# Kernel tuning notes

Measured on AMD Instinct MI355X. Metric: run time of the kernel, lower is better.

## Reference

```python
import jax, jax.numpy as jnp
import numpy as np

B, N, C = 16, 256, 2048
CLASSES = (16, 5, 5)
H = len(CLASSES)
EPS = 1e-5


def setup_inputs() -> dict:
    key = jax.random.key(0)
    ks = iter(jax.random.split(key, 32))
    d = {}
    d["features"] = jax.random.normal(next(ks), (B, N, C), dtype=jnp.float32)
    # 3 hidden conv layers per head; 3x3 conv on 1x1 spatial == linear with center tap.
    # Stack the H heads' weights: [H, C_out, C_in].
    std = 1.0 / np.sqrt(C)
    for i in (1, 2, 3):
        d[f"W{i}"] = jax.random.normal(next(ks), (H, C, C), dtype=jnp.float32) * std
        d[f"g{i}"] = 1.0 + 0.1 * jax.random.normal(next(ks), (H, C), dtype=jnp.float32)
        d[f"b{i}"] = 0.1 * jax.random.normal(next(ks), (H, C), dtype=jnp.float32)
        d[f"m{i}"] = 0.1 * jax.random.normal(next(ks), (H, C), dtype=jnp.float32)
        d[f"v{i}"] = jax.random.uniform(next(ks), (H, C), dtype=jnp.float32, minval=0.5, maxval=1.5)
    # Final 1x1 conv per head: [c_i, C] weight + [c_i] bias (output dims differ per head).
    for h, c in enumerate(CLASSES):
        d[f"Wf{h}"] = jax.random.normal(next(ks), (c, C), dtype=jnp.float32) * std
        d[f"bf{h}"] = 0.1 * jax.random.normal(next(ks), (c,), dtype=jnp.float32)
    return d


def _bn_relu(y, g, b, m, v):
    # y: [H, M, C]; per-head inference-mode BN folded to scale/shift, then ReLU.
    scale = g / jnp.sqrt(v + EPS)          # [H, C]
    shift = b - m * scale                  # [H, C]
    return jax.nn.relu(y * scale[:, None, :] + shift[:, None, :])


def reference(features, W1, g1, b1, m1, v1, W2, g2, b2, m2, v2, W3, g3, b3, m3, v3,
              Wf0, bf0, Wf1, bf1, Wf2, bf2):
    Bs, Ns, Cs = features.shape
    x = features.reshape(Bs * Ns, Cs)                       # [M, C]
    y = jnp.einsum("mc,hdc->hmd", x, W1)                    # [H, M, C]
    y = _bn_relu(y, g1, b1, m1, v1)
    y = jnp.einsum("hmc,hdc->hmd", y, W2)
    y = _bn_relu(y, g2, b2, m2, v2)
    y = jnp.einsum("hmc,hdc->hmd", y, W3)
    y = _bn_relu(y, g3, b3, m3, v3)
    outs = [y[h] @ Wf.T + bf for h, (Wf, bf) in enumerate([(Wf0, bf0), (Wf1, bf1), (Wf2, bf2)])]
    cl = jnp.concatenate(outs, axis=-1)                     # [M, sum(classes)]
    return cl.reshape(Bs, Ns, cl.shape[-1])
```

## Files before the change

### kernel.cpp

```cpp
#include <hip/hip_runtime.h>
#include <hip/hip_bf16.h>

typedef __attribute__((ext_vector_type(8))) short short8;
typedef __attribute__((ext_vector_type(4))) float f32x4;

#define BN_EPS 1e-5f
#define MROWS 4096
#define CDIM 2048

#define SB() __builtin_amdgcn_sched_barrier(0)

__device__ __forceinline__ void gload_lds16(const void* g, void* l) {
  __builtin_amdgcn_global_load_lds(
      (const __attribute__((address_space(1))) void*)g,
      (__attribute__((address_space(3))) void*)l, 16, 0, 0);
}

__global__ __launch_bounds__(256) void cvt_f32_bf16(const float* __restrict__ in,
                                                    unsigned short* __restrict__ out,
                                                    int n4) {
  int idx = blockIdx.x * blockDim.x + threadIdx.x;
  int stride = gridDim.x * blockDim.x;
  for (int i = idx; i < n4; i += stride) {
    float4 vv = ((const float4*)in)[i];
    __hip_bfloat16 h0 = __float2bfloat16(vv.x);
    __hip_bfloat16 h1 = __float2bfloat16(vv.y);
    __hip_bfloat16 h2 = __float2bfloat16(vv.z);
    __hip_bfloat16 h3 = __float2bfloat16(vv.w);
    ushort4 o;
    o.x = *(unsigned short*)&h0;
    o.y = *(unsigned short*)&h1;
    o.z = *(unsigned short*)&h2;
    o.w = *(unsigned short*)&h3;
    ((ushort4*)out)[i] = o;
  }
}

__global__ __launch_bounds__(512, 4) void gemm128_bn_relu(
    const __hip_bfloat16* __restrict__ A, long long a_hstride,
    const __hip_bfloat16* __restrict__ W,
    const float* __restrict__ gp, const float* __restrict__ bp,
    const float* __restrict__ mp, const float* __restrict__ vp,
    __hip_bfloat16* __restrict__ out)
{
  __shared__ __hip_bfloat16 sm[36864];

  const int tid  = threadIdx.x;
  const int w    = tid >> 6;
  const int lane = tid & 63;

  const int bid = blockIdx.x;
  const int swz = (bid & 7) * 96 + (bid >> 3);
  const int h   = swz >> 8;
  const int rem = swz & 255;
  const int mt  = rem >> 3;
  const int nt  = rem & 7;

  const __hip_bfloat16* Abase = A + (size_t)h * (size_t)a_hstride + (size_t)(mt * 128) * CDIM;
  const __hip_bfloat16* Bbase = W + ((size_t)h * CDIM + (size_t)(nt * 256)) * CDIM;

  const int rowA = tid >> 2;
  const int chA  = (tid & 3) ^ ((rowA >> 1) & 3);
  const __hip_bfloat16* aSrc  = Abase + (size_t)rowA * CDIM + chA * 8;
  const __hip_bfloat16* bSrc0 = Bbase + (size_t)rowA * CDIM + chA * 8;
  const __hip_bfloat16* bSrc1 = bSrc0 + (size_t)128 * CDIM;

  const int wm = w >> 2, wn = w & 3;
  const int fr = lane & 15, fg = lane >> 4;
  const int cadj  = (fg ^ ((fr >> 1) & 3)) * 8;
  const int abase = (wm * 64 + fr) * 32 + cadj;
  const int bbase = 4096 + (wn * 64 + fr) * 32 + cadj;

  auto STAGE = [&](int off, int t) {
    __hip_bfloat16* dp = &sm[off + tid * 8];
    gload_lds16(aSrc  + t * 32, dp);
    gload_lds16(bSrc0 + t * 32, dp + 4096);
    gload_lds16(bSrc1 + t * 32, dp + 8192);
  };

  f32x4 acc[4][4] = {};

  STAGE(0, 0);
  STAGE(12288, 1);
  asm volatile("s_waitcnt vmcnt(3)" ::: "memory");
  SB();
  __builtin_amdgcn_s_barrier();
  SB();

  int oc = 0, on = 12288, os = 24576;
  for (int t = 0; t < 64; ++t) {
    if (t + 2 < 64) STAGE(os, t + 2);
    SB();
    short8 af[4], bf_[4];
#pragma unroll
    for (int i = 0; i < 4; ++i) af[i]  = *(const short8*)&sm[oc + abase + i * 512];
#pragma unroll
    for (int j = 0; j < 4; ++j) bf_[j] = *(const short8*)&sm[oc + bbase + j * 512];
    __builtin_amdgcn_s_setprio(1);
#pragma unroll
    for (int i = 0; i < 4; ++i)
#pragma unroll
      for (int j = 0; j < 4; ++j)
        acc[i][j] = __builtin_amdgcn_mfma_f32_16x16x32_bf16(af[i], bf_[j], acc[i][j], 0, 0, 0);
    __builtin_amdgcn_s_setprio(0);
    SB();
    if (t < 63) {
      if (t + 2 < 64) { asm volatile("s_waitcnt vmcnt(3)" ::: "memory"); }
      else            { asm volatile("s_waitcnt vmcnt(0)" ::: "memory"); }
      SB();
      __builtin_amdgcn_s_barrier();
      SB();
    }
    const int tmp = oc; oc = on; on = os; os = tmp;
  }

  const float* gh = gp + h * CDIM;
  const float* bh = bp + h * CDIM;
  const float* mh = mp + h * CDIM;
  const float* vh = vp + h * CDIM;
  const int colBase = nt * 256 + wn * 64 + fr;
  const int rowBase = mt * 128 + wm * 64 + fg * 4;
#pragma unroll
  for (int j = 0; j < 4; ++j) {
    const int col = colBase + j * 16;
    const float sc = gh[col] / sqrtf(vh[col] + BN_EPS);
    const float sh = bh[col] - mh[col] * sc;
#pragma unroll
    for (int i = 0; i < 4; ++i) {
      const int row = rowBase + i * 16;
#pragma unroll
      for (int rr = 0; rr < 4; ++rr) {
        float val = acc[i][j][rr] * sc + sh;
        val = val > 0.f ? val : 0.f;
        out[((size_t)h * MROWS + row + rr) * CDIM + col] = __float2bfloat16(val);
      }
    }
  }
}

__global__ __launch_bounds__(256) void pack_wf(
    const float* __restrict__ Wf0, const float* __restrict__ Wf1,
    const float* __restrict__ Wf2, __hip_bfloat16* __restrict__ Wfb) {
  int idx = blockIdx.x * 256 + threadIdx.x;
  if (idx >= 3 * 16 * CDIM) return;
  int h = idx / (16 * CDIM);
  int rem = idx - h * 16 * CDIM;
  int j = rem / CDIM;
  int k = rem - j * CDIM;
  float v = 0.f;
  if (h == 0)            v = Wf0[j * CDIM + k];
  else if (h == 1)       { if (j < 5) v = Wf1[j * CDIM + k]; }
  else                   { if (j < 5) v = Wf2[j * CDIM + k]; }
  Wfb[idx] = __float2bfloat16(v);
}

__global__ __launch_bounds__(512) void final_mfma(
    const __hip_bfloat16* __restrict__ act,
    const __hip_bfloat16* __restrict__ Wfb,
    const float* __restrict__ bf0, const float* __restrict__ bf1,
    const float* __restrict__ bf2, float* __restrict__ out)
{
  __shared__ float red[8][3][256];
  const int tid  = threadIdx.x;
  const int w    = tid >> 6;
  const int lane = tid & 63;
  const int r0   = blockIdx.x * 16;
  const int fr   = lane & 15;
  const int fk   = (lane >> 4) * 8;
  const int kbase = w * 256 + fk;

  f32x4 acc[3] = {};
  const __hip_bfloat16* aRow = act + (size_t)(r0 + fr) * CDIM + kbase;
  const __hip_bfloat16* bRow = Wfb + (size_t)fr * CDIM + kbase;
#pragma unroll
  for (int ks = 0; ks < 8; ++ks) {
    const int k = ks * 32;
#pragma unroll
    for (int h = 0; h < 3; ++h) {
      short8 a = *(const short8*)(aRow + (size_t)h * MROWS * CDIM + k);
      short8 b = *(const short8*)(bRow + h * 16 * CDIM + k);
      acc[h] = __builtin_amdgcn_mfma_f32_16x16x32_bf16(a, b, acc[h], 0, 0, 0);
    }
  }

  const int rb = (lane >> 4) * 4;
#pragma unroll
  for (int h = 0; h < 3; ++h)
#pragma unroll
    for (int r = 0; r < 4; ++r)
      red[w][h][(rb + r) * 16 + fr] = acc[h][r];
  __syncthreads();

  for (int e = tid; e < 768; e += 512) {
    const int h = e >> 8, idx = e & 255;
    const int row = idx >> 4, col = idx & 15;
    float s = 0.f;
#pragma unroll
    for (int w2 = 0; w2 < 8; ++w2) s += red[w2][h][idx];
    float* orow = out + (size_t)(r0 + row) * 26;
    if (h == 0)                 orow[col]      = s + bf0[col];
    else if (h == 1) { if (col < 5) orow[16 + col] = s + bf1[col]; }
    else             { if (col < 5) orow[21 + col] = s + bf2[col]; }
  }
}

extern "C" void kernel_launch(void* const* d_in, const int* in_sizes, int n_in,
                              void* d_out, int out_size, void* d_ws, size_t ws_size,
                              hipStream_t stream) {
  const float* feat = (const float*)d_in[0];
  const float* W1 = (const float*)d_in[1];
  const float* g1 = (const float*)d_in[2];
  const float* b1 = (const float*)d_in[3];
  const float* m1 = (const float*)d_in[4];
  const float* v1 = (const float*)d_in[5];
  const float* W2 = (const float*)d_in[6];
  const float* g2 = (const float*)d_in[7];
  const float* b2 = (const float*)d_in[8];
  const float* m2 = (const float*)d_in[9];
  const float* v2 = (const float*)d_in[10];
  const float* W3 = (const float*)d_in[11];
  const float* g3 = (const float*)d_in[12];
  const float* b3 = (const float*)d_in[13];
  const float* m3 = (const float*)d_in[14];
  const float* v3 = (const float*)d_in[15];
  const float* Wf0 = (const float*)d_in[16];
  const float* bf0 = (const float*)d_in[17];
  const float* Wf1 = (const float*)d_in[18];
  const float* bf1 = (const float*)d_in[19];
  const float* Wf2 = (const float*)d_in[20];
  const float* bf2 = (const float*)d_in[21];
  float* out = (float*)d_out;

  char* ws = (char*)d_ws;
  __hip_bfloat16* wbuf = (__hip_bfloat16*)ws;
  __hip_bfloat16* actA = (__hip_bfloat16*)(ws + 25165824);
  __hip_bfloat16* actB = (__hip_bfloat16*)(ws + 25165824 + 50331648);
  __hip_bfloat16* xb   = actB;
  __hip_bfloat16* Wfb  = wbuf;

  const int nW4 = (3 * CDIM * CDIM) / 4;
  const int nX4 = (MROWS * CDIM) / 4;
  const long long hstride = (long long)MROWS * CDIM;

  cvt_f32_bf16<<<2048, 256, 0, stream>>>(feat, (unsigned short*)xb, nX4);

  cvt_f32_bf16<<<2048, 256, 0, stream>>>(W1, (unsigned short*)wbuf, nW4);
  gemm128_bn_relu<<<768, 512, 0, stream>>>(xb, 0LL, wbuf, g1, b1, m1, v1, actA);

  cvt_f32_bf16<<<2048, 256, 0, stream>>>(W2, (unsigned short*)wbuf, nW4);
  gemm128_bn_relu<<<768, 512, 0, stream>>>(actA, hstride, wbuf, g2, b2, m2, v2, actB);

  cvt_f32_bf16<<<2048, 256, 0, stream>>>(W3, (unsigned short*)wbuf, nW4);
  gemm128_bn_relu<<<768, 512, 0, stream>>>(actB, hstride, wbuf, g3, b3, m3, v3, actA);

  pack_wf<<<384, 256, 0, stream>>>(Wf0, Wf1, Wf2, Wfb);
  final_mfma<<<256, 512, 0, stream>>>(actA, Wfb, bf0, bf1, bf2, out);
}
```

Measured before the change: 389.8 us.

## Widen GEMM K-tile to 64 and interleave LDS fragment loads with MFMA

The main bf16 GEMM now stages K-tiles of 64 instead of 32, which halves the number of barrier iterations, and it uses a new XOR swizzle for the 64-wide rows. Within each iteration the work is split into four MFMA groups, with LDS fragment reads and global-to-LDS prefetches placed between them so data movement overlaps compute. The next tile's first fragments are loaded right after the barrier. In exchange, LDS use doubles to 144 KB per block and the occupancy hint drops to 2 blocks per CU, so fewer waves are resident to hide latency.

```diff
diff --git a/kernel.cpp b/kernel.cpp
--- a/kernel.cpp
+++ b/kernel.cpp
@@ -7,6 +7,7 @@
 #define BN_EPS 1e-5f
 #define MROWS 4096
 #define CDIM 2048
+#define NKT 32
 
 #define SB() __builtin_amdgcn_sched_barrier(0)
 
@@ -36,14 +37,14 @@
   }
 }
 
-__global__ __launch_bounds__(512, 4) void gemm128_bn_relu(
+__global__ __launch_bounds__(512, 2) void gemm128_ring(
     const __hip_bfloat16* __restrict__ A, long long a_hstride,
     const __hip_bfloat16* __restrict__ W,
     const float* __restrict__ gp, const float* __restrict__ bp,
     const float* __restrict__ mp, const float* __restrict__ vp,
     __hip_bfloat16* __restrict__ out)
 {
-  __shared__ __hip_bfloat16 sm[36864];
+  __shared__ __hip_bfloat16 sm[73728];
 
   const int tid  = threadIdx.x;
   const int w    = tid >> 6;
@@ -59,56 +60,89 @@
   const __hip_bfloat16* Abase = A + (size_t)h * (size_t)a_hstride + (size_t)(mt * 128) * CDIM;
   const __hip_bfloat16* Bbase = W + ((size_t)h * CDIM + (size_t)(nt * 256)) * CDIM;
 
-  const int rowA = tid >> 2;
-  const int chA  = (tid & 3) ^ ((rowA >> 1) & 3);
-  const __hip_bfloat16* aSrc  = Abase + (size_t)rowA * CDIM + chA * 8;
-  const __hip_bfloat16* bSrc0 = Bbase + (size_t)rowA * CDIM + chA * 8;
-  const __hip_bfloat16* bSrc1 = bSrc0 + (size_t)128 * CDIM;
+  const int row0 = tid >> 3;
+  const int ch0  = (tid & 7) ^ (row0 & 7);
+  const __hip_bfloat16* aSrc = Abase + (size_t)row0 * CDIM + ch0 * 8;
+  const __hip_bfloat16* bSrc = Bbase + (size_t)row0 * CDIM + ch0 * 8;
 
   const int wm = w >> 2, wn = w & 3;
   const int fr = lane & 15, fg = lane >> 4;
-  const int cadj  = (fg ^ ((fr >> 1) & 3)) * 8;
-  const int abase = (wm * 64 + fr) * 32 + cadj;
-  const int bbase = 4096 + (wn * 64 + fr) * 32 + cadj;
-
-  auto STAGE = [&](int off, int t) {
-    __hip_bfloat16* dp = &sm[off + tid * 8];
-    gload_lds16(aSrc  + t * 32, dp);
-    gload_lds16(bSrc0 + t * 32, dp + 4096);
-    gload_lds16(bSrc1 + t * 32, dp + 8192);
+  const int offs0 = fr * 64 + ((fg ^ (fr & 7)) << 3);
+  const int offs1 = fr * 64 + (((fg + 4) ^ (fr & 7)) << 3);
+  const int aoffs0 = wm * 4096 + offs0;
+  const int aoffs1 = wm * 4096 + offs1;
+  const int boffs0 = 8192 + wn * 4096 + offs0;
+  const int boffs1 = 8192 + wn * 4096 + offs1;
+
+  auto SA = [&](int buf, int t) {
+    __hip_bfloat16* dp = &sm[buf + tid * 8];
+    gload_lds16(aSrc + t * 64, dp);
+    gload_lds16(aSrc + (size_t)64 * CDIM + t * 64, dp + 4096);
   };
+  auto SB0 = [&](int buf, int t) {
+    __hip_bfloat16* dp = &sm[buf + 8192 + tid * 8];
+    gload_lds16(bSrc + t * 64, dp);
+    gload_lds16(bSrc + (size_t)64 * CDIM + t * 64, dp + 4096);
+  };
+  auto SB1 = [&](int buf, int t) {
+    __hip_bfloat16* dp = &sm[buf + 8192 + 8192 + tid * 8];
+    gload_lds16(bSrc + (size_t)128 * CDIM + t * 64, dp);
+    gload_lds16(bSrc + (size_t)192 * CDIM + t * 64, dp + 4096);
+  };
 
   f32x4 acc[4][4] = {};
-
-  STAGE(0, 0);
-  STAGE(12288, 1);
-  asm volatile("s_waitcnt vmcnt(3)" ::: "memory");
+  short8 Af[4], Ap[4], B0[2], B1[2], B0p[2], B1p[2];
+
+#define LDA4(dst, base)                                                  \
+  _Pragma("unroll") for (int i_ = 0; i_ < 4; ++i_)                       \
+    dst[i_] = *(const short8*)&sm[(base) + i_ * 1024];
+#define LDB2(dst, base, j0)                                              \
+  _Pragma("unroll") for (int j_ = 0; j_ < 2; ++j_)                       \
+    dst[j_] = *(const short8*)&sm[(base) + ((j0) + j_) * 1024];
+
+#define MFMA_G(joff, Aset, Bset)                                         \
+  __builtin_amdgcn_s_setprio(1);                                         \
+  _Pragma("unroll") for (int i_ = 0; i_ < 4; ++i_)                       \
+  _Pragma("unroll") for (int j_ = 0; j_ < 2; ++j_)                       \
+    acc[i_][j_ + joff] = __builtin_amdgcn_mfma_f32_16x16x32_bf16(        \
+        Aset[i_], Bset[j_], acc[i_][j_ + joff], 0, 0, 0);                \
+  __builtin_amdgcn_s_setprio(0);
+
+  SA(0, 0); SB0(0, 0); SB1(0, 0);
+  SA(24576, 1); SB0(24576, 1); SB1(24576, 1);
+  asm volatile("s_waitcnt vmcnt(6)" ::: "memory");
   SB();
   __builtin_amdgcn_s_barrier();
   SB();
-
-  int oc = 0, on = 12288, os = 24576;
-  for (int t = 0; t < 64; ++t) {
-    if (t + 2 < 64) STAGE(os, t + 2);
+  LDA4(Af, 0 + aoffs0);
+  LDB2(B0, 0 + boffs0, 0);
+  LDB2(B1, 0 + boffs0, 2);
+  SB();
+
+  int oc = 0, on = 24576, os = 49152;
+  for (int t = 0; t < NKT; ++t) {
+    MFMA_G(0, Af, B0); SB();
+    LDB2(B0p, oc + boffs1, 0); SB();
+    MFMA_G(2, Af, B1); SB();
+    LDA4(Ap, oc + aoffs1);
+    if (t + 2 < NKT) SA(os, t + 2);
     SB();
-    short8 af[4], bf_[4];
-#pragma unroll
-    for (int i = 0; i < 4; ++i) af[i]  = *(const short8*)&sm[oc + abase + i * 512];
-#pragma unroll
-    for (int j = 0; j < 4; ++j) bf_[j] = *(const short8*)&sm[oc + bbase + j * 512];
-    __builtin_amdgcn_s_setprio(1);
-#pragma unroll
-    for (int i = 0; i < 4; ++i)
-#pragma unroll
-      for (int j = 0; j < 4; ++j)
-        acc[i][j] = __builtin_amdgcn_mfma_f32_16x16x32_bf16(af[i], bf_[j], acc[i][j], 0, 0, 0);
-    __builtin_amdgcn_s_setprio(0);
+    MFMA_G(0, Ap, B0p); SB();
+    LDB2(B1p, oc + boffs1, 2);
+    if (t + 2 < NKT) SB0(os, t + 2);
     SB();
-    if (t < 63) {
-      if (t + 2 < 64) { asm volatile("s_waitcnt vmcnt(3)" ::: "memory"); }
-      else            { asm volatile("s_waitcnt vmcnt(0)" ::: "memory"); }
+    MFMA_G(2, Ap, B1p); SB();
+    if (t + 2 < NKT) SB1(os, t + 2);
+    SB();
+    if (t < NKT - 1) {
+      if (t + 2 < NKT) { asm volatile("s_waitcnt vmcnt(6)" ::: "memory"); }
+      else             { asm volatile("s_waitcnt vmcnt(0)" ::: "memory"); }
       SB();
       __builtin_amdgcn_s_barrier();
+      SB();
+      LDA4(Af, on + aoffs0);
+      LDB2(B0, on + boffs0, 0);
+      LDB2(B1, on + boffs0, 2);
       SB();
     }
     const int tmp = oc; oc = on; on = os; os = tmp;
@@ -245,13 +279,13 @@
   cvt_f32_bf16<<<2048, 256, 0, stream>>>(feat, (unsigned short*)xb, nX4);
 
   cvt_f32_bf16<<<2048, 256, 0, stream>>>(W1, (unsigned short*)wbuf, nW4);
-  gemm128_bn_relu<<<768, 512, 0, stream>>>(xb, 0LL, wbuf, g1, b1, m1, v1, actA);
+  gemm128_ring<<<768, 512, 0, stream>>>(xb, 0LL, wbuf, g1, b1, m1, v1, actA);
 
   cvt_f32_bf16<<<2048, 256, 0, stream>>>(W2, (unsigned short*)wbuf, nW4);
-  gemm128_bn_relu<<<768, 512, 0, stream>>>(actA, hstride, wbuf, g2, b2, m2, v2, actB);
+  gemm128_ring<<<768, 512, 0, stream>>>(actA, hstride, wbuf, g2, b2, m2, v2, actB);
 
   cvt_f32_bf16<<<2048, 256, 0, stream>>>(W3, (unsigned short*)wbuf, nW4);
-  gemm128_bn_relu<<<768, 512, 0, stream>>>(actB, hstride, wbuf, g3, b3, m3, v3, actA);
+  gemm128_ring<<<768, 512, 0, stream>>>(actB, hstride, wbuf, g3, b3, m3, v3, actA);
 
   pack_wf<<<384, 256, 0, stream>>>(Wf0, Wf1, Wf2, Wfb);
   final_mfma<<<256, 512, 0, stream>>>(actA, Wfb, bf0, bf1, bf2, out);
```

Result: faster. 363.4 us (-6.8%).

## Load GEMM B operand directly from global into registers, stage only A in LDS

Applied to the files above, without the earlier changes.

Restructures the main GEMM so the weight (B) fragments are loaded directly from global memory into registers per wave and double-buffered across K steps, while only the A tile goes through LDS with a triple buffer. K step doubles to 64 with a new XOR swizzle, and A fragment LDS reads are interleaved with MFMA groups. The goal is to cut LDS traffic and footprint for B and overlap loads with compute. In exchange, register pressure rises (launch bounds drop to 2 waves per SIMD) and B global loads are uncoalesced 16-byte row reads that rely on cache.

```diff
diff --git a/kernel.cpp b/kernel.cpp
--- a/kernel.cpp
+++ b/kernel.cpp
@@ -7,6 +7,7 @@
 #define BN_EPS 1e-5f
 #define MROWS 4096
 #define CDIM 2048
+#define NKT 32
 
 #define SB() __builtin_amdgcn_sched_barrier(0)
 
@@ -36,14 +37,14 @@
   }
 }
 
-__global__ __launch_bounds__(512, 4) void gemm128_bn_relu(
+__global__ __launch_bounds__(512, 2) void gemm_bdir(
     const __hip_bfloat16* __restrict__ A, long long a_hstride,
     const __hip_bfloat16* __restrict__ W,
     const float* __restrict__ gp, const float* __restrict__ bp,
     const float* __restrict__ mp, const float* __restrict__ vp,
     __hip_bfloat16* __restrict__ out)
 {
-  __shared__ __hip_bfloat16 sm[36864];
+  __shared__ __hip_bfloat16 sm[24576];
 
   const int tid  = threadIdx.x;
   const int w    = tid >> 6;
@@ -57,61 +58,85 @@
   const int nt  = rem & 7;
 
   const __hip_bfloat16* Abase = A + (size_t)h * (size_t)a_hstride + (size_t)(mt * 128) * CDIM;
-  const __hip_bfloat16* Bbase = W + ((size_t)h * CDIM + (size_t)(nt * 256)) * CDIM;
-
-  const int rowA = tid >> 2;
-  const int chA  = (tid & 3) ^ ((rowA >> 1) & 3);
-  const __hip_bfloat16* aSrc  = Abase + (size_t)rowA * CDIM + chA * 8;
-  const __hip_bfloat16* bSrc0 = Bbase + (size_t)rowA * CDIM + chA * 8;
-  const __hip_bfloat16* bSrc1 = bSrc0 + (size_t)128 * CDIM;
+
+  const int row0 = tid >> 3;
+  const int ch0  = (tid & 7) ^ (row0 & 7);
+  const __hip_bfloat16* aSrc = Abase + (size_t)row0 * CDIM + ch0 * 8;
 
   const int wm = w >> 2, wn = w & 3;
   const int fr = lane & 15, fg = lane >> 4;
-  const int cadj  = (fg ^ ((fr >> 1) & 3)) * 8;
-  const int abase = (wm * 64 + fr) * 32 + cadj;
-  const int bbase = 4096 + (wn * 64 + fr) * 32 + cadj;
-
-  auto STAGE = [&](int off, int t) {
-    __hip_bfloat16* dp = &sm[off + tid * 8];
-    gload_lds16(aSrc  + t * 32, dp);
-    gload_lds16(bSrc0 + t * 32, dp + 4096);
-    gload_lds16(bSrc1 + t * 32, dp + 8192);
+  const int offs0 = fr * 64 + ((fg ^ (fr & 7)) << 3);
+  const int offs1 = fr * 64 + (((fg + 4) ^ (fr & 7)) << 3);
+
+  const __hip_bfloat16* bP = W +
+      ((size_t)h * CDIM + (size_t)(nt * 256 + wn * 64 + fr)) * CDIM + fg * 8;
+
+  auto SA_ = [&](int slotOff, int t) {
+    __hip_bfloat16* dp = &sm[slotOff + tid * 8];
+    gload_lds16(aSrc + t * 64, dp);
+    gload_lds16(aSrc + (size_t)64 * CDIM + t * 64, dp + 4096);
   };
 
   f32x4 acc[4][4] = {};
-
-  STAGE(0, 0);
-  STAGE(12288, 1);
-  asm volatile("s_waitcnt vmcnt(3)" ::: "memory");
+  short8 Af[4], Ap[4], Bx[4][2], By[4][2];
+
+#define LDA4(dst, base)                                                  \
+  _Pragma("unroll") for (int i_ = 0; i_ < 4; ++i_)                       \
+    dst[i_] = *(const short8*)&sm[(base) + i_ * 1024];
+
+#define ISSUE_B(Bset, t1)                                                \
+  _Pragma("unroll") for (int j_ = 0; j_ < 4; ++j_) {                     \
+    Bset[j_][0] = *(const short8*)(bP + (size_t)j_ * 16 * CDIM + (t1) * 64);      \
+    Bset[j_][1] = *(const short8*)(bP + (size_t)j_ * 16 * CDIM + (t1) * 64 + 32); \
+  }
+
+#define MFMA_G(Aset, Bset, ks, j0)                                       \
+  __builtin_amdgcn_s_setprio(1);                                         \
+  _Pragma("unroll") for (int i_ = 0; i_ < 4; ++i_)                       \
+  _Pragma("unroll") for (int j_ = 0; j_ < 2; ++j_)                       \
+    acc[i_][j_ + j0] = __builtin_amdgcn_mfma_f32_16x16x32_bf16(          \
+        Aset[i_], Bset[j_ + j0][ks], acc[i_][j_ + j0], 0, 0, 0);         \
+  __builtin_amdgcn_s_setprio(0);
+
+#define BODY(Bc, Bn, t)                                                  \
+  {                                                                      \
+    MFMA_G(Af, Bc, 0, 0);                                                \
+    SB();                                                                \
+    if ((t) + 1 < NKT) { ISSUE_B(Bn, (t) + 1); }                         \
+    SB();                                                                \
+    MFMA_G(Af, Bc, 0, 2);                                                \
+    SB();                                                                \
+    LDA4(Ap, oc + wm * 4096 + offs1);                                    \
+    SB();                                                                \
+    MFMA_G(Ap, Bc, 1, 0);                                                \
+    SB();                                                                \
+    if ((t) < NKT - 1) {                                                 \
+      asm volatile("s_waitcnt vmcnt(8)" ::: "memory");                   \
+      SB();                                                              \
+      __builtin_amdgcn_s_barrier();                                      \
+      SB();                                                              \
+      if ((t) + 2 < NKT) SA_(os, (t) + 2);                               \
+      LDA4(Af, on + wm * 4096 + offs0);                                  \
+    }                                                                    \
+    SB();                                                                \
+    MFMA_G(Ap, Bc, 1, 2);                                                \
+    SB();                                                                \
+    int tmp_ = oc; oc = on; on = os; os = tmp_;                          \
+  }
+
+  SA_(0, 0); SA_(8192, 1);
+  ISSUE_B(Bx, 0);
+  asm volatile("s_waitcnt vmcnt(10)" ::: "memory");
   SB();
   __builtin_amdgcn_s_barrier();
   SB();
-
-  int oc = 0, on = 12288, os = 24576;
-  for (int t = 0; t < 64; ++t) {
-    if (t + 2 < 64) STAGE(os, t + 2);
-    SB();
-    short8 af[4], bf_[4];
-#pragma unroll
-    for (int i = 0; i < 4; ++i) af[i]  = *(const short8*)&sm[oc + abase + i * 512];
-#pragma unroll
-    for (int j = 0; j < 4; ++j) bf_[j] = *(const short8*)&sm[oc + bbase + j * 512];
-    __builtin_amdgcn_s_setprio(1);
-#pragma unroll
-    for (int i = 0; i < 4; ++i)
-#pragma unroll
-      for (int j = 0; j < 4; ++j)
-        acc[i][j] = __builtin_amdgcn_mfma_f32_16x16x32_bf16(af[i], bf_[j], acc[i][j], 0, 0, 0);
-    __builtin_amdgcn_s_setprio(0);
-    SB();
-    if (t < 63) {
-      if (t + 2 < 64) { asm volatile("s_waitcnt vmcnt(3)" ::: "memory"); }
-      else            { asm volatile("s_waitcnt vmcnt(0)" ::: "memory"); }
-      SB();
-      __builtin_amdgcn_s_barrier();
-      SB();
-    }
-    const int tmp = oc; oc = on; on = os; os = tmp;
+  LDA4(Af, 0 + wm * 4096 + offs0);
+  SB();
+
+  int oc = 0, on = 8192, os = 16384;
+  for (int t = 0; t < NKT; t += 2) {
+    BODY(Bx, By, t);
+    BODY(By, Bx, t + 1);
   }
 
   const float* gh = gp + h * CDIM;
@@ -245,13 +270,13 @@
   cvt_f32_bf16<<<2048, 256, 0, stream>>>(feat, (unsigned short*)xb, nX4);
 
   cvt_f32_bf16<<<2048, 256, 0, stream>>>(W1, (unsigned short*)wbuf, nW4);
-  gemm128_bn_relu<<<768, 512, 0, stream>>>(xb, 0LL, wbuf, g1, b1, m1, v1, actA);
+  gemm_bdir<<<768, 512, 0, stream>>>(xb, 0LL, wbuf, g1, b1, m1, v1, actA);
 
   cvt_f32_bf16<<<2048, 256, 0, stream>>>(W2, (unsigned short*)wbuf, nW4);
-  gemm128_bn_relu<<<768, 512, 0, stream>>>(actA, hstride, wbuf, g2, b2, m2, v2, actB);
+  gemm_bdir<<<768, 512, 0, stream>>>(actA, hstride, wbuf, g2, b2, m2, v2, actB);
 
   cvt_f32_bf16<<<2048, 256, 0, stream>>>(W3, (unsigned short*)wbuf, nW4);
-  gemm128_bn_relu<<<768, 512, 0, stream>>>(actB, hstride, wbuf, g3, b3, m3, v3, actA);
+  gemm_bdir<<<768, 512, 0, stream>>>(actB, hstride, wbuf, g3, b3, m3, v3, actA);
 
   pack_wf<<<384, 256, 0, stream>>>(Wf0, Wf1, Wf2, Wfb);
   final_mfma<<<256, 512, 0, stream>>>(actA, Wfb, bf0, bf1, bf2, out);
```

Result: slower. 705.2 us (+80.9%).
